# Performance work log

Hardware: AMD Instinct MI355X
Metric: run time of the kernel (lower is better)

## Reference

```python
import jax, jax.numpy as jnp
import numpy as np

# Static problem constants (must match setup_inputs)
NUM_GRAPHS = 64      # batch_size = int(batch[-1]) + 1
PTS_PER_GRAPH = 512
RATIO = 16           # centroids per graph
HEADS = 4
IN_CH = 64           # = out_channels per head (concat=False -> mean over heads)
NEG_SLOPE = 0.2


def setup_inputs() -> dict:
    key = jax.random.key(0)
    ks = jax.random.split(key, 8)
    N = NUM_GRAPHS * PTS_PER_GRAPH
    x = jax.random.normal(ks[0], (N, IN_CH), dtype=jnp.float32)
    edge_index = jnp.zeros((2, 2), dtype=jnp.int64)  # unused by forward
    batch = (jnp.arange(N) // PTS_PER_GRAPH).astype(jnp.int64)
    xcent_base = jax.random.normal(ks[1], (RATIO, IN_CH), dtype=jnp.float32)
    W_l = jax.random.normal(ks[2], (IN_CH, HEADS * IN_CH), dtype=jnp.float32) / np.sqrt(IN_CH)
    b_l = jax.random.normal(ks[3], (HEADS * IN_CH,), dtype=jnp.float32) * 0.01
    W_r = jax.random.normal(ks[4], (IN_CH, HEADS * IN_CH), dtype=jnp.float32) / np.sqrt(IN_CH)
    b_r = jax.random.normal(ks[5], (HEADS * IN_CH,), dtype=jnp.float32) * 0.01
    att = jax.random.normal(ks[6], (HEADS, IN_CH), dtype=jnp.float32) / np.sqrt(IN_CH)
    bias = jax.random.normal(ks[7], (IN_CH,), dtype=jnp.float32) * 0.01
    return {"x": x, "edge_index": edge_index, "batch": batch,
            "xcent_base": xcent_base, "W_l": W_l, "b_l": b_l,
            "W_r": W_r, "b_r": b_r, "att": att, "bias": bias}


def _bipart_pool(x, batch, xcent_base, W_l, b_l, W_r, b_r, att, bias):
    N = x.shape[0]
    B = NUM_GRAPHS
    Nc = B * RATIO  # number of centroid (target) nodes

    # Dense bipartite edges: each source node -> all RATIO centroids of its graph.
    src = jnp.repeat(jnp.arange(N, dtype=jnp.int32), RATIO)                     # [E]
    dst = jnp.tile(jnp.arange(RATIO, dtype=jnp.int32), N) \
        + jnp.repeat(batch.astype(jnp.int32), RATIO) * RATIO                    # [E]

    # PyG GATv2Conv(add_self_loops=True): remove src==dst edges, then add
    # self loops (i,i) for i < min(N_src, N_dst) = Nc. Keep static shapes by
    # masking the removed edges instead of deleting them.
    self_idx = jnp.arange(Nc, dtype=jnp.int32)
    src_f = jnp.concatenate([src, self_idx])
    dst_f = jnp.concatenate([dst, self_idx])
    drop = jnp.concatenate([src == dst, jnp.zeros((Nc,), dtype=bool)])          # [E+Nc]

    # Linear projections (source and target sides)
    x_l = (x @ W_l + b_l).reshape(N, HEADS, IN_CH)                              # [N,H,C]
    xcent = jnp.tile(xcent_base, (B, 1))                                        # [Nc,IN]
    x_r = (xcent @ W_r + b_r).reshape(Nc, HEADS, IN_CH)                         # [Nc,H,C]

    # GATv2 attention: leaky_relu(x_i + x_j) . att, softmax per target node
    xj = x_l[src_f]                                                             # [E',H,C]
    g = jax.nn.leaky_relu(xj + x_r[dst_f], NEG_SLOPE)
    alpha = jnp.einsum('ehc,hc->eh', g, att)                                    # [E',H]
    alpha = jnp.where(drop[:, None], jnp.float32(-1e30), alpha)
    amax = jax.ops.segment_max(alpha, dst_f, num_segments=Nc)                   # [Nc,H]
    e = jnp.exp(alpha - amax[dst_f])
    den = jax.ops.segment_sum(e, dst_f, num_segments=Nc)                        # [Nc,H]
    w = e / den[dst_f]                                                          # [E',H]

    out = jax.ops.segment_sum(w[..., None] * xj, dst_f, num_segments=Nc)        # [Nc,H,C]
    out = out.mean(axis=1) + bias                                               # concat=False -> mean heads
    return out.reshape(B, RATIO, IN_CH)


def reference(x, edge_index, batch, xcent_base, W_l, b_l, W_r, b_r, att, bias):
    xcent = _bipart_pool(x, batch, xcent_base, W_l, b_l, W_r, b_r, att, bias)
    batchcent = jnp.repeat(jnp.arange(NUM_GRAPHS, dtype=jnp.int64), RATIO)
    return xcent, batchcent
```

## Files before the change

### kernel.cpp

```cpp
#include <hip/hip_runtime.h>
#include <hip/hip_bf16.h>

#define PTS    512
#define NG     64
#define RATIO  16
#define CH     64
#define NC     1024

__global__ __launch_bounds__(512) void ka(
    const float* __restrict__ x, const float* __restrict__ xcb,
    const float* __restrict__ W_l, const float* __restrict__ b_l,
    const float* __restrict__ W_r, const float* __restrict__ b_r,
    const float* __restrict__ att, float* __restrict__ part)
{
    __shared__ float sW[64][64];
    __shared__ float s_att[64];
    __shared__ float s_bl[64];
    __shared__ float s_alpha[16 * 512];
    __shared__ float s_aself[16], s_den[16], s_eself[16], s_sxr[16];
    __shared__ float s_pool[3072];

    const int b   = blockIdx.x >> 2;
    const int h   = blockIdx.x & 3;
    const int tid = threadIdx.x;

    if (tid < 64) {
        s_att[tid] = att[h * 64 + tid];
        s_bl[tid]  = b_l[h * 64 + tid];
    }
    for (int idx = tid; idx < 4096; idx += 512) {
        int k = idx >> 6, c = idx & 63;
        sW[k][c] = W_l[k * 256 + h * 64 + c];
    }
    for (int idx = tid; idx < 1024; idx += 512)
        s_pool[idx] = xcb[idx];
    for (int idx = tid; idx < 1024; idx += 512)
        s_pool[1024 + idx] = x[b * 1024 + idx];
    __syncthreads();

    for (int idx = tid; idx < 1024; idx += 512) {
        int r = idx >> 6, c = idx & 63;
        float acc = b_r[h * 64 + c];
        for (int k = 0; k < 64; ++k)
            acc = fmaf(s_pool[r * 64 + k], W_r[k * 256 + h * 64 + c], acc);
        s_pool[2048 + idx] = acc;
    }
    __syncthreads();
    if (tid < 16) {
        float s = 0.f;
        for (int c = 0; c < 64; ++c)
            s = fmaf(s_pool[2048 + tid * 64 + c], s_att[c], s);
        s_sxr[tid] = s;
    }
    __syncthreads();

    {
        const int row = tid;
        const float4* xp = (const float4*)(x + (size_t)(b * PTS + row) * CH);
        float xl[64];
#pragma unroll
        for (int c = 0; c < 64; ++c) xl[c] = s_bl[c];
        for (int k4 = 0; k4 < 16; ++k4) {
            float4 u = xp[k4];
            float xk[4] = {u.x, u.y, u.z, u.w};
#pragma unroll
            for (int j = 0; j < 4; ++j) {
                float xv = xk[j];
                const float* wr = &sW[k4 * 4 + j][0];
#pragma unroll
                for (int cq = 0; cq < 16; ++cq) {
                    float4 w = *(const float4*)(wr + cq * 4);
                    xl[cq * 4 + 0] = fmaf(xv, w.x, xl[cq * 4 + 0]);
                    xl[cq * 4 + 1] = fmaf(xv, w.y, xl[cq * 4 + 1]);
                    xl[cq * 4 + 2] = fmaf(xv, w.z, xl[cq * 4 + 2]);
                    xl[cq * 4 + 3] = fmaf(xv, w.w, xl[cq * 4 + 3]);
                }
            }
        }
        float sxl = 0.f;
#pragma unroll
        for (int c = 0; c < 64; ++c) sxl = fmaf(xl[c], s_att[c], sxl);

#pragma unroll
        for (int r = 0; r < 16; ++r) {
            float acc = 0.f;
            const float* xrr = s_pool + 2048 + r * 64;
#pragma unroll
            for (int cq = 0; cq < 16; ++cq) {
                float4 xr4 = *(const float4*)(xrr + cq * 4);
                float4 at4 = *(const float4*)(s_att + cq * 4);
                acc = fmaf(fabsf(xl[cq * 4 + 0] + xr4.x), at4.x, acc);
                acc = fmaf(fabsf(xl[cq * 4 + 1] + xr4.y), at4.y, acc);
                acc = fmaf(fabsf(xl[cq * 4 + 2] + xr4.z), at4.z, acc);
                acc = fmaf(fabsf(xl[cq * 4 + 3] + xr4.w), at4.w, acc);
            }
            s_alpha[r * 512 + row] = 0.6f * (sxl + s_sxr[r]) + 0.4f * acc;
        }
    }

    {
        int r = tid >> 5, cp = tid & 31;
        float a0 = s_bl[2 * cp], a1 = s_bl[2 * cp + 1];
#pragma unroll
        for (int k = 0; k < 64; ++k) {
            float xv = s_pool[1024 + r * 64 + k];
            float2 w = *(const float2*)&sW[k][2 * cp];
            a0 = fmaf(xv, w.x, a0);
            a1 = fmaf(xv, w.y, a1);
        }
        __syncthreads();
        s_pool[1024 + r * 64 + 2 * cp]     = a0;
        s_pool[1024 + r * 64 + 2 * cp + 1] = a1;
    }
    __syncthreads();
    if (tid < 16) {
        int r = tid;
        float sxl = 0.f, acc = 0.f;
        for (int c = 0; c < 64; ++c) {
            float v = s_pool[1024 + r * 64 + c];
            sxl = fmaf(v, s_att[c], sxl);
            acc = fmaf(fabsf(v + s_pool[2048 + r * 64 + c]), s_att[c], acc);
        }
        s_aself[r] = 0.6f * (sxl + s_sxr[r]) + 0.4f * acc;
    }
    __syncthreads();

    {
        int r = tid >> 5, lg = tid & 31;
        float m = -1e30f;
#pragma unroll
        for (int j = 0; j < 16; ++j) {
            int i = lg + j * 32;
            float a = s_alpha[r * 512 + i];
            if (b == 0 && i == r) a = -1e30f;
            m = fmaxf(m, a);
        }
#pragma unroll
        for (int off = 16; off >= 1; off >>= 1)
            m = fmaxf(m, __shfl_xor(m, off));
        m = fmaxf(m, s_aself[r]);
        float d = 0.f;
#pragma unroll
        for (int j = 0; j < 16; ++j) {
            int i = lg + j * 32;
            float a = s_alpha[r * 512 + i];
            float e = (b == 0 && i == r) ? 0.f : __expf(a - m);
            s_alpha[r * 512 + i] = e;
            d += e;
        }
#pragma unroll
        for (int off = 16; off >= 1; off >>= 1)
            d += __shfl_xor(d, off);
        if (lg == 0) {
            float es = __expf(s_aself[r] - m);
            s_eself[r] = es;
            s_den[r] = d + es;
        }
    }

    float y0 = 0.f, y1 = 0.f;
    const int r5 = tid >> 5, kp5 = tid & 31;
    for (int chk = 0; chk < 16; ++chk) {
        __syncthreads();
        {
            float4 v = ((const float4*)(x + (size_t)b * 32768 + chk * 2048))[tid];
            int dst = (tid < 256) ? 4 * tid : 4 * tid + 1024;
            *(float4*)&s_pool[dst] = v;
        }
        __syncthreads();
#pragma unroll 4
        for (int i = 0; i < 16; ++i) {
            float e = s_alpha[r5 * 512 + chk * 32 + i];
            float2 xv = *(const float2*)&s_pool[i * 64 + 2 * kp5];
            y0 = fmaf(e, xv.x, y0);
            y1 = fmaf(e, xv.y, y1);
        }
#pragma unroll 4
        for (int i = 0; i < 16; ++i) {
            float e = s_alpha[r5 * 512 + chk * 32 + 16 + i];
            float2 xv = *(const float2*)&s_pool[2048 + i * 64 + 2 * kp5];
            y0 = fmaf(e, xv.x, y0);
            y1 = fmaf(e, xv.y, y1);
        }
    }
    __syncthreads();
    s_pool[r5 * 64 + 2 * kp5]     = y0;
    s_pool[r5 * 64 + 2 * kp5 + 1] = y1;
    __syncthreads();

    {
        int r = tid >> 5, cp = tid & 31;
        float den = s_den[r];
        float es  = s_eself[r];
        float o0 = (den - es) * s_bl[2 * cp];
        float o1 = (den - es) * s_bl[2 * cp + 1];
#pragma unroll
        for (int k = 0; k < 64; ++k) {
            float yv = s_pool[r * 64 + k];
            float2 w = *(const float2*)&sW[k][2 * cp];
            o0 = fmaf(yv, w.x, o0);
            o1 = fmaf(yv, w.y, o1);
        }
        o0 = fmaf(es, s_pool[1024 + r * 64 + 2 * cp],     o0);
        o1 = fmaf(es, s_pool[1024 + r * 64 + 2 * cp + 1], o1);
        float inv = 1.f / den;
        *(float2*)(part + ((size_t)(b * RATIO + r) * 4 + h) * 64 + 2 * cp) =
            make_float2(o0 * inv, o1 * inv);
    }
}

__global__ __launch_bounds__(256) void kb(const float* __restrict__ part,
                                          const float* __restrict__ bias,
                                          float* __restrict__ out)
{
    int idx = blockIdx.x * 256 + threadIdx.x;
    int ch = idx & 63;
    const float* p = part + (size_t)(idx >> 6) * 256 + ch;
    out[idx] = 0.25f * (p[0] + p[64] + p[128] + p[192]) + bias[ch];
    if (idx < NC)
        out[NC * CH + idx] = (float)(idx >> 4);
}

extern "C" void kernel_launch(void* const* d_in, const int* in_sizes, int n_in,
                              void* d_out, int out_size, void* d_ws, size_t ws_size,
                              hipStream_t stream) {
    (void)in_sizes; (void)n_in; (void)out_size; (void)ws_size;
    const float* x    = (const float*)d_in[0];
    const float* xcb  = (const float*)d_in[3];
    const float* W_l  = (const float*)d_in[4];
    const float* b_l  = (const float*)d_in[5];
    const float* W_r  = (const float*)d_in[6];
    const float* b_r  = (const float*)d_in[7];
    const float* att  = (const float*)d_in[8];
    const float* bias = (const float*)d_in[9];
    float* out = (float*)d_out;

    float* part = (float*)d_ws;

    hipLaunchKernelGGL(ka, dim3(NG * 4), dim3(512), 0, stream,
                       x, xcb, W_l, b_l, W_r, b_r, att, part);
    hipLaunchKernelGGL(kb, dim3(256), dim3(256), 0, stream, part, bias, out);
}
```

Before: 137.4 us.

## Split attention kernel into score and aggregation kernels with register tiling

Splits the single fused kernel in two. The first computes attention logits with 256 threads, each handling two source rows, and writes them and the needed x_l rows to workspace. The second runs the softmax and a register-tiled 4x4 weighted aggregation over a padded x tile, then applies the W_l projection. The aim is to reduce LDS pressure and shared-array conflicts and to improve FMA reuse. The cost is an extra launch and a global round trip for the 8 MB of logits, plus much higher register pressure in the first kernel.

```diff
diff --git a/kernel.cpp b/kernel.cpp
--- a/kernel.cpp
+++ b/kernel.cpp
@@ -1,5 +1,4 @@
 #include <hip/hip_runtime.h>
-#include <hip/hip_bf16.h>
 
 #define PTS    512
 #define NG     64
@@ -7,209 +6,229 @@
 #define CH     64
 #define NC     1024
 
-__global__ __launch_bounds__(512) void ka(
+__global__ __launch_bounds__(256) void k1(
     const float* __restrict__ x, const float* __restrict__ xcb,
     const float* __restrict__ W_l, const float* __restrict__ b_l,
     const float* __restrict__ W_r, const float* __restrict__ b_r,
-    const float* __restrict__ att, float* __restrict__ part)
+    const float* __restrict__ att,
+    float* __restrict__ aws, float* __restrict__ xlws)
 {
-    __shared__ float sW[64][64];
-    __shared__ float s_att[64];
-    __shared__ float s_bl[64];
-    __shared__ float s_alpha[16 * 512];
-    __shared__ float s_aself[16], s_den[16], s_eself[16], s_sxr[16];
-    __shared__ float s_pool[3072];
-
-    const int b   = blockIdx.x >> 2;
-    const int h   = blockIdx.x & 3;
+    __shared__ float sW[4096];
+    __shared__ float s_xc[1024];
+    __shared__ float s_xr[1024];
+    __shared__ float s_att[64], s_bl[64], s_sxr[16];
+
+    const int b = blockIdx.x >> 2, h = blockIdx.x & 3;
     const int tid = threadIdx.x;
 
-    if (tid < 64) {
-        s_att[tid] = att[h * 64 + tid];
-        s_bl[tid]  = b_l[h * 64 + tid];
-    }
-    for (int idx = tid; idx < 4096; idx += 512) {
-        int k = idx >> 6, c = idx & 63;
-        sW[k][c] = W_l[k * 256 + h * 64 + c];
-    }
-    for (int idx = tid; idx < 1024; idx += 512)
-        s_pool[idx] = xcb[idx];
-    for (int idx = tid; idx < 1024; idx += 512)
-        s_pool[1024 + idx] = x[b * 1024 + idx];
-    __syncthreads();
-
-    for (int idx = tid; idx < 1024; idx += 512) {
+    if (tid < 64) { s_att[tid] = att[h * 64 + tid]; s_bl[tid] = b_l[h * 64 + tid]; }
+    for (int idx = tid; idx < 4096; idx += 256)
+        sW[idx] = W_l[(idx >> 6) * 256 + h * 64 + (idx & 63)];
+    for (int idx = tid; idx < 1024; idx += 256) s_xc[idx] = xcb[idx];
+    __syncthreads();
+
+    for (int idx = tid; idx < 1024; idx += 256) {
         int r = idx >> 6, c = idx & 63;
         float acc = b_r[h * 64 + c];
         for (int k = 0; k < 64; ++k)
-            acc = fmaf(s_pool[r * 64 + k], W_r[k * 256 + h * 64 + c], acc);
-        s_pool[2048 + idx] = acc;
+            acc = fmaf(s_xc[r * 64 + k], W_r[k * 256 + h * 64 + c], acc);
+        s_xr[idx] = acc;
     }
     __syncthreads();
     if (tid < 16) {
         float s = 0.f;
-        for (int c = 0; c < 64; ++c)
-            s = fmaf(s_pool[2048 + tid * 64 + c], s_att[c], s);
+        for (int c = 0; c < 64; ++c) s = fmaf(s_xr[tid * 64 + c], s_att[c], s);
         s_sxr[tid] = s;
     }
     __syncthreads();
 
+    const int i0 = tid, i1 = tid + 256;
+    const float4* xp0 = (const float4*)(x + ((size_t)b * PTS + i0) * CH);
+    const float4* xp1 = (const float4*)(x + ((size_t)b * PTS + i1) * CH);
+    float xl0[64], xl1[64];
+#pragma unroll
+    for (int c = 0; c < 64; ++c) { xl0[c] = s_bl[c]; xl1[c] = s_bl[c]; }
+
+    for (int k4 = 0; k4 < 16; ++k4) {
+        float4 u0 = xp0[k4], u1 = xp1[k4];
+        float a0[4] = {u0.x, u0.y, u0.z, u0.w};
+        float a1[4] = {u1.x, u1.y, u1.z, u1.w};
+#pragma unroll
+        for (int j = 0; j < 4; ++j) {
+            const float* wr = &sW[(k4 * 4 + j) * 64];
+#pragma unroll
+            for (int cq = 0; cq < 16; ++cq) {
+                float4 w = *(const float4*)(wr + cq * 4);
+                xl0[cq*4+0] = fmaf(a0[j], w.x, xl0[cq*4+0]);
+                xl0[cq*4+1] = fmaf(a0[j], w.y, xl0[cq*4+1]);
+                xl0[cq*4+2] = fmaf(a0[j], w.z, xl0[cq*4+2]);
+                xl0[cq*4+3] = fmaf(a0[j], w.w, xl0[cq*4+3]);
+                xl1[cq*4+0] = fmaf(a1[j], w.x, xl1[cq*4+0]);
+                xl1[cq*4+1] = fmaf(a1[j], w.y, xl1[cq*4+1]);
+                xl1[cq*4+2] = fmaf(a1[j], w.z, xl1[cq*4+2]);
+                xl1[cq*4+3] = fmaf(a1[j], w.w, xl1[cq*4+3]);
+            }
+        }
+    }
+
+    float sxl0 = 0.f, sxl1 = 0.f;
+    float ac0[16], ac1[16];
+#pragma unroll
+    for (int r = 0; r < 16; ++r) { ac0[r] = 0.f; ac1[r] = 0.f; }
+#pragma unroll
+    for (int cq = 0; cq < 16; ++cq) {
+        float4 at = *(const float4*)&s_att[cq * 4];
+        sxl0 = fmaf(xl0[cq*4+0], at.x, sxl0); sxl0 = fmaf(xl0[cq*4+1], at.y, sxl0);
+        sxl0 = fmaf(xl0[cq*4+2], at.z, sxl0); sxl0 = fmaf(xl0[cq*4+3], at.w, sxl0);
+        sxl1 = fmaf(xl1[cq*4+0], at.x, sxl1); sxl1 = fmaf(xl1[cq*4+1], at.y, sxl1);
+        sxl1 = fmaf(xl1[cq*4+2], at.z, sxl1); sxl1 = fmaf(xl1[cq*4+3], at.w, sxl1);
+#pragma unroll
+        for (int r = 0; r < 16; ++r) {
+            float4 xr4 = *(const float4*)&s_xr[r * 64 + cq * 4];
+            ac0[r] = fmaf(fabsf(xl0[cq*4+0] + xr4.x), at.x, ac0[r]);
+            ac0[r] = fmaf(fabsf(xl0[cq*4+1] + xr4.y), at.y, ac0[r]);
+            ac0[r] = fmaf(fabsf(xl0[cq*4+2] + xr4.z), at.z, ac0[r]);
+            ac0[r] = fmaf(fabsf(xl0[cq*4+3] + xr4.w), at.w, ac0[r]);
+            ac1[r] = fmaf(fabsf(xl1[cq*4+0] + xr4.x), at.x, ac1[r]);
+            ac1[r] = fmaf(fabsf(xl1[cq*4+1] + xr4.y), at.y, ac1[r]);
+            ac1[r] = fmaf(fabsf(xl1[cq*4+2] + xr4.z), at.z, ac1[r]);
+            ac1[r] = fmaf(fabsf(xl1[cq*4+3] + xr4.w), at.w, ac1[r]);
+        }
+    }
+
+    float* ap = aws + (size_t)(b * 4 + h) * 8192;
+#pragma unroll
+    for (int r = 0; r < 16; ++r) {
+        ap[r * 512 + i0] = 0.6f * (sxl0 + s_sxr[r]) + 0.4f * ac0[r];
+        ap[r * 512 + i1] = 0.6f * (sxl1 + s_sxr[r]) + 0.4f * ac1[r];
+    }
+
+    if (b < 2) {
+        float* d0 = xlws + ((size_t)(b * PTS + i0) * 4 + h) * 64;
+        float* d1 = xlws + ((size_t)(b * PTS + i1) * 4 + h) * 64;
+#pragma unroll
+        for (int c = 0; c < 64; c += 4) {
+            *(float4*)(d0 + c) = make_float4(xl0[c], xl0[c+1], xl0[c+2], xl0[c+3]);
+            *(float4*)(d1 + c) = make_float4(xl1[c], xl1[c+1], xl1[c+2], xl1[c+3]);
+        }
+    }
+}
+
+__global__ __launch_bounds__(512) void k2(
+    const float* __restrict__ x, const float* __restrict__ W_l,
+    const float* __restrict__ b_l, const float* __restrict__ aws,
+    const float* __restrict__ xlws, float* __restrict__ part)
+{
+    __shared__ float s_e[8192];
+    __shared__ float sW[4096];
+    __shared__ float s_x[2176];
+    __shared__ float s_den[16], s_es[16];
+
+    const int b = blockIdx.x >> 2, h = blockIdx.x & 3;
+    const int tid = threadIdx.x;
+
+    const float* ap = aws + (size_t)(b * 4 + h) * 8192;
+    for (int idx = tid; idx < 8192; idx += 512) s_e[idx] = ap[idx];
+    for (int idx = tid; idx < 4096; idx += 512)
+        sW[idx] = W_l[(idx >> 6) * 256 + h * 64 + (idx & 63)];
+    __syncthreads();
+
     {
-        const int row = tid;
-        const float4* xp = (const float4*)(x + (size_t)(b * PTS + row) * CH);
-        float xl[64];
-#pragma unroll
-        for (int c = 0; c < 64; ++c) xl[c] = s_bl[c];
-        for (int k4 = 0; k4 < 16; ++k4) {
-            float4 u = xp[k4];
-            float xk[4] = {u.x, u.y, u.z, u.w};
-#pragma unroll
-            for (int j = 0; j < 4; ++j) {
-                float xv = xk[j];
-                const float* wr = &sW[k4 * 4 + j][0];
-#pragma unroll
-                for (int cq = 0; cq < 16; ++cq) {
-                    float4 w = *(const float4*)(wr + cq * 4);
-                    xl[cq * 4 + 0] = fmaf(xv, w.x, xl[cq * 4 + 0]);
-                    xl[cq * 4 + 1] = fmaf(xv, w.y, xl[cq * 4 + 1]);
-                    xl[cq * 4 + 2] = fmaf(xv, w.z, xl[cq * 4 + 2]);
-                    xl[cq * 4 + 3] = fmaf(xv, w.w, xl[cq * 4 + 3]);
-                }
-            }
-        }
-        float sxl = 0.f;
-#pragma unroll
-        for (int c = 0; c < 64; ++c) sxl = fmaf(xl[c], s_att[c], sxl);
-
-#pragma unroll
-        for (int r = 0; r < 16; ++r) {
-            float acc = 0.f;
-            const float* xrr = s_pool + 2048 + r * 64;
-#pragma unroll
-            for (int cq = 0; cq < 16; ++cq) {
-                float4 xr4 = *(const float4*)(xrr + cq * 4);
-                float4 at4 = *(const float4*)(s_att + cq * 4);
-                acc = fmaf(fabsf(xl[cq * 4 + 0] + xr4.x), at4.x, acc);
-                acc = fmaf(fabsf(xl[cq * 4 + 1] + xr4.y), at4.y, acc);
-                acc = fmaf(fabsf(xl[cq * 4 + 2] + xr4.z), at4.z, acc);
-                acc = fmaf(fabsf(xl[cq * 4 + 3] + xr4.w), at4.w, acc);
-            }
-            s_alpha[r * 512 + row] = 0.6f * (sxl + s_sxr[r]) + 0.4f * acc;
-        }
-    }
-
-    {
-        int r = tid >> 5, cp = tid & 31;
-        float a0 = s_bl[2 * cp], a1 = s_bl[2 * cp + 1];
-#pragma unroll
-        for (int k = 0; k < 64; ++k) {
-            float xv = s_pool[1024 + r * 64 + k];
-            float2 w = *(const float2*)&sW[k][2 * cp];
-            a0 = fmaf(xv, w.x, a0);
-            a1 = fmaf(xv, w.y, a1);
-        }
-        __syncthreads();
-        s_pool[1024 + r * 64 + 2 * cp]     = a0;
-        s_pool[1024 + r * 64 + 2 * cp + 1] = a1;
-    }
-    __syncthreads();
-    if (tid < 16) {
-        int r = tid;
-        float sxl = 0.f, acc = 0.f;
-        for (int c = 0; c < 64; ++c) {
-            float v = s_pool[1024 + r * 64 + c];
-            sxl = fmaf(v, s_att[c], sxl);
-            acc = fmaf(fabsf(v + s_pool[2048 + r * 64 + c]), s_att[c], acc);
-        }
-        s_aself[r] = 0.6f * (sxl + s_sxr[r]) + 0.4f * acc;
-    }
-    __syncthreads();
-
-    {
-        int r = tid >> 5, lg = tid & 31;
-        float m = -1e30f;
+        const int r = tid >> 5, lg = tid & 31;
+        const int snode = b * 16 + r;
+        const float a_self =
+            aws[(size_t)((snode >> 9) * 4 + h) * 8192 + r * 512 + (snode & 511)];
+        float m = a_self;
 #pragma unroll
         for (int j = 0; j < 16; ++j) {
             int i = lg + j * 32;
-            float a = s_alpha[r * 512 + i];
+            float a = s_e[r * 512 + i];
             if (b == 0 && i == r) a = -1e30f;
             m = fmaxf(m, a);
         }
 #pragma unroll
-        for (int off = 16; off >= 1; off >>= 1)
-            m = fmaxf(m, __shfl_xor(m, off));
-        m = fmaxf(m, s_aself[r]);
+        for (int off = 16; off >= 1; off >>= 1) m = fmaxf(m, __shfl_xor(m, off));
         float d = 0.f;
 #pragma unroll
         for (int j = 0; j < 16; ++j) {
             int i = lg + j * 32;
-            float a = s_alpha[r * 512 + i];
+            float a = s_e[r * 512 + i];
             float e = (b == 0 && i == r) ? 0.f : __expf(a - m);
-            s_alpha[r * 512 + i] = e;
+            s_e[r * 512 + i] = e;
             d += e;
         }
 #pragma unroll
-        for (int off = 16; off >= 1; off >>= 1)
-            d += __shfl_xor(d, off);
+        for (int off = 16; off >= 1; off >>= 1) d += __shfl_xor(d, off);
         if (lg == 0) {
-            float es = __expf(s_aself[r] - m);
-            s_eself[r] = es;
+            float es = __expf(a_self - m);
+            s_es[r] = es;
             s_den[r] = d + es;
         }
     }
 
-    float y0 = 0.f, y1 = 0.f;
-    const int r5 = tid >> 5, kp5 = tid & 31;
+    const int rg = tid >> 7;
+    const int sl = (tid >> 4) & 7;
+    const int qd = tid & 15;
+    float y4[4][4];
+#pragma unroll
+    for (int i = 0; i < 4; ++i)
+#pragma unroll
+        for (int j = 0; j < 4; ++j) y4[i][j] = 0.f;
+
+    const float* xb = x + (size_t)b * PTS * CH;
     for (int chk = 0; chk < 16; ++chk) {
         __syncthreads();
         {
-            float4 v = ((const float4*)(x + (size_t)b * 32768 + chk * 2048))[tid];
-            int dst = (tid < 256) ? 4 * tid : 4 * tid + 1024;
-            *(float4*)&s_pool[dst] = v;
+            float4 v = ((const float4*)(xb + chk * 2048))[tid];
+            int rI = tid >> 4, cI = (tid & 15) * 4;
+            *(float4*)&s_x[rI * 68 + cI] = v;
         }
         __syncthreads();
-#pragma unroll 4
-        for (int i = 0; i < 16; ++i) {
-            float e = s_alpha[r5 * 512 + chk * 32 + i];
-            float2 xv = *(const float2*)&s_pool[i * 64 + 2 * kp5];
-            y0 = fmaf(e, xv.x, y0);
-            y1 = fmaf(e, xv.y, y1);
-        }
-#pragma unroll 4
-        for (int i = 0; i < 16; ++i) {
-            float e = s_alpha[r5 * 512 + chk * 32 + 16 + i];
-            float2 xv = *(const float2*)&s_pool[2048 + i * 64 + 2 * kp5];
-            y0 = fmaf(e, xv.x, y0);
-            y1 = fmaf(e, xv.y, y1);
-        }
-    }
-    __syncthreads();
-    s_pool[r5 * 64 + 2 * kp5]     = y0;
-    s_pool[r5 * 64 + 2 * kp5 + 1] = y1;
-    __syncthreads();
-
-    {
-        int r = tid >> 5, cp = tid & 31;
-        float den = s_den[r];
-        float es  = s_eself[r];
-        float o0 = (den - es) * s_bl[2 * cp];
-        float o1 = (den - es) * s_bl[2 * cp + 1];
-#pragma unroll
-        for (int k = 0; k < 64; ++k) {
-            float yv = s_pool[r * 64 + k];
-            float2 w = *(const float2*)&sW[k][2 * cp];
-            o0 = fmaf(yv, w.x, o0);
-            o1 = fmaf(yv, w.y, o1);
-        }
-        o0 = fmaf(es, s_pool[1024 + r * 64 + 2 * cp],     o0);
-        o1 = fmaf(es, s_pool[1024 + r * 64 + 2 * cp + 1], o1);
-        float inv = 1.f / den;
-        *(float2*)(part + ((size_t)(b * RATIO + r) * 4 + h) * 64 + 2 * cp) =
-            make_float2(o0 * inv, o1 * inv);
-    }
-}
-
-__global__ __launch_bounds__(256) void kb(const float* __restrict__ part,
+#pragma unroll
+        for (int ii = 0; ii < 4; ++ii) {
+            int i = sl * 4 + ii;
+            float4 xv = *(const float4*)&s_x[i * 68 + qd * 4];
+#pragma unroll
+            for (int rr = 0; rr < 4; ++rr) {
+                float e = s_e[(rg * 4 + rr) * 512 + chk * 32 + i];
+                y4[rr][0] = fmaf(e, xv.x, y4[rr][0]);
+                y4[rr][1] = fmaf(e, xv.y, y4[rr][1]);
+                y4[rr][2] = fmaf(e, xv.z, y4[rr][2]);
+                y4[rr][3] = fmaf(e, xv.w, y4[rr][3]);
+            }
+        }
+    }
+    __syncthreads();
+#pragma unroll
+    for (int rr = 0; rr < 4; ++rr)
+        *(float4*)&s_e[sl * 1024 + (rg * 4 + rr) * 64 + qd * 4] =
+            make_float4(y4[rr][0], y4[rr][1], y4[rr][2], y4[rr][3]);
+    __syncthreads();
+
+    float* s_y = s_x;
+    for (int o = tid; o < 1024; o += 512) {
+        float s = 0.f;
+#pragma unroll
+        for (int slj = 0; slj < 8; ++slj) s += s_e[slj * 1024 + o];
+        s_y[o] = s;
+    }
+    __syncthreads();
+
+    for (int o = tid; o < 1024; o += 512) {
+        int r = o >> 6, ch = o & 63;
+        float acc = 0.f;
+#pragma unroll
+        for (int k = 0; k < 64; ++k)
+            acc = fmaf(s_y[r * 64 + k], sW[k * 64 + ch], acc);
+        float den = s_den[r], es = s_es[r];
+        float bl = b_l[h * 64 + ch];
+        float xs = xlws[((size_t)(b * 16 + r) * 4 + h) * 64 + ch];
+        part[((size_t)(b * 16 + r) * 4 + h) * 64 + ch] =
+            (acc + (den - es) * bl + es * xs) / den;
+    }
+}
+
+__global__ __launch_bounds__(256) void k3(const float* __restrict__ part,
                                           const float* __restrict__ bias,
                                           float* __restrict__ out)
 {
@@ -235,9 +254,14 @@
     const float* bias = (const float*)d_in[9];
     float* out = (float*)d_out;
 
-    float* part = (float*)d_ws;
-
-    hipLaunchKernelGGL(ka, dim3(NG * 4), dim3(512), 0, stream,
-                       x, xcb, W_l, b_l, W_r, b_r, att, part);
-    hipLaunchKernelGGL(kb, dim3(256), dim3(256), 0, stream, part, bias, out);
-}
+    char* ws = (char*)d_ws;
+    float* aws  = (float*)ws;
+    float* xlws = (float*)(ws + (size_t)8  * 1024 * 1024);
+    float* part = (float*)(ws + (size_t)9  * 1024 * 1024);
+
+    hipLaunchKernelGGL(k1, dim3(NG * 4), dim3(256), 0, stream,
+                       x, xcb, W_l, b_l, W_r, b_r, att, aws, xlws);
+    hipLaunchKernelGGL(k2, dim3(NG * 4), dim3(512), 0, stream,
+                       x, W_l, b_l, aws, xlws, part);
+    hipLaunchKernelGGL(k3, dim3(256), dim3(256), 0, stream, part, bias, out);
+}
```

After: 131.4 us. 4.4% less time.
